# Kernel tuning notes

Measured on AMD Instinct MI355X. Metric: run time of the kernel, lower is better.

The kernel has to match this reference:

```python
import jax, jax.numpy as jnp
import numpy as np

N_NODES = 100_000
N_EDGES = 1_600_000
IN_C, OUT_C = 128, 64


def setup_inputs() -> dict:
    key = jax.random.key(0)
    k1, k2, k3, k4 = jax.random.split(key, 4)
    x = jax.random.normal(k1, (N_NODES, IN_C), dtype=jnp.float32)
    # xavier_uniform with relu gain sqrt(2)
    gain = float(np.sqrt(2.0))
    bound = gain * float(np.sqrt(6.0 / (IN_C + OUT_C)))
    weight = jax.random.uniform(k2, (IN_C, OUT_C), minval=-bound, maxval=bound, dtype=jnp.float32)
    bias = jnp.zeros((OUT_C,), dtype=jnp.float32)
    src = jax.random.randint(k3, (N_EDGES,), 0, N_NODES, dtype=jnp.int32)
    dst = jax.random.randint(k4, (N_EDGES,), 0, N_NODES, dtype=jnp.int32)
    return {"x": x, "weight": weight, "bias": bias, "src": src, "dst": dst}


def reference(x, weight, bias, src, dst):
    # DGL GraphConv, norm='both'.
    n = x.shape[0]
    ones = jnp.ones(src.shape, dtype=x.dtype)
    deg_out = jax.ops.segment_sum(ones, src, num_segments=n)  # source out-degree
    deg_in = jax.ops.segment_sum(ones, dst, num_segments=n)   # destination in-degree
    norm_src = jnp.maximum(deg_out, 1.0) ** -0.5
    norm_dst = jnp.maximum(deg_in, 1.0) ** -0.5
    h = x * norm_src[:, None]          # [N, IN]
    # in_channels > out_channels: apply weight before aggregation (DGL fast path)
    h = h @ weight                      # [N, OUT]
    msg = h[src]                        # [E, OUT] gather
    agg = jax.ops.segment_sum(msg, dst, num_segments=n)  # [N, OUT] scatter-add
    return agg * norm_dst[:, None] + bias
```

## Files before the change

kernel.cpp:

```cpp
#include <hip/hip_runtime.h>
#include <hip/hip_bf16.h>

#define N_NODES 100000
#define N_EDGES 1600000
#define IN_C    128
#define OUT_C   64

#define SLOT_W 48
#define CAP    47

#define GEMM_BLK 512
#define FILL_BLK ((N_EDGES + 255) / 256)

typedef __bf16 bf16x8 __attribute__((ext_vector_type(8)));
typedef float  f32x4  __attribute__((ext_vector_type(4)));

#define DEGS_OFF  0
#define CNT_OFF   400000
#define SLOT_OFF  800000
#define H_OFF     20000000

__global__ __launch_bounds__(256) void fused_fill_gemm(
    const float* __restrict__ x, const float* __restrict__ w,
    const int* __restrict__ src, const int* __restrict__ dst,
    int* __restrict__ degs, int* __restrict__ cnt, int* __restrict__ slots,
    __bf16* __restrict__ h) {
  if (blockIdx.x >= GEMM_BLK) {
    const int i = (blockIdx.x - GEMM_BLK) * 256 + threadIdx.x;
    if (i < N_EDGES) {
      const int s = src[i];
      const int d = dst[i];
      atomicAdd(&degs[s], 1);
      const int pos = atomicAdd(&cnt[d], 1);
      if (pos < CAP) slots[d * SLOT_W + pos] = s;
    }
    return;
  }

  const int lane = threadIdx.x & 63;
  const int l15 = lane & 15;
  const int q = lane >> 4;
  const int wave = blockIdx.x * 4 + (threadIdx.x >> 6);
  const int n_waves = GEMM_BLK * 4;
  const int n_groups = N_NODES / 16;

  bf16x8 bfrag[4][4];
#pragma unroll
  for (int kc = 0; kc < 4; ++kc) {
#pragma unroll
    for (int t = 0; t < 4; ++t) {
      bf16x8 tmp;
#pragma unroll
      for (int j = 0; j < 8; ++j)
        tmp[j] = (__bf16)w[(kc * 32 + q * 8 + j) * OUT_C + t * 16 + l15];
      bfrag[kc][t] = tmp;
    }
  }

  for (int g = wave; g < n_groups; g += n_waves) {
    const int n0 = g * 16;
    const float* xp = x + (long)(n0 + l15) * IN_C + q * 8;

    f32x4 acc[4];
#pragma unroll
    for (int t = 0; t < 4; ++t) {
      f32x4 z = {0.f, 0.f, 0.f, 0.f};
      acc[t] = z;
    }

#pragma unroll
    for (int kc = 0; kc < 4; ++kc) {
      f32x4 u = *(const f32x4*)(xp + kc * 32);
      f32x4 v = *(const f32x4*)(xp + kc * 32 + 4);
      bf16x8 a;
#pragma unroll
      for (int j = 0; j < 4; ++j) {
        a[j] = (__bf16)u[j];
        a[4 + j] = (__bf16)v[j];
      }
#pragma unroll
      for (int t = 0; t < 4; ++t)
        acc[t] = __builtin_amdgcn_mfma_f32_16x16x32_bf16(a, bfrag[kc][t], acc[t], 0, 0, 0);
    }

#pragma unroll
    for (int r = 0; r < 4; ++r) {
      const int row = n0 + q * 4 + r;
#pragma unroll
      for (int t = 0; t < 4; ++t)
        h[(long)row * OUT_C + t * 16 + l15] = (__bf16)acc[t][r];
    }
  }
}

__global__ __launch_bounds__(256) void scale_kernel(
    __bf16* __restrict__ h, const int* __restrict__ degs) {
  int tid = blockIdx.x * 256 + threadIdx.x;
  if (tid >= N_NODES * 8) return;
  int n = tid >> 3;
  int c8 = (tid & 7) * 8;
  int d = degs[n];
  float s = rsqrtf((float)(d < 1 ? 1 : d));
  bf16x8* p = (bf16x8*)(h + (long)n * OUT_C + c8);
  bf16x8 v = *p;
#pragma unroll
  for (int k = 0; k < 8; ++k) v[k] = (__bf16)((float)v[k] * s);
  *p = v;
}

__global__ __launch_bounds__(256) void aggregate_kernel(
    const __bf16* __restrict__ h, const int* __restrict__ cnt,
    const int* __restrict__ slots, const float* __restrict__ bias,
    float* __restrict__ out) {
  const int node = blockIdx.x * 4 + (threadIdx.x >> 6);
  if (node >= N_NODES) return;
  const int lane = threadIdx.x & 63;
  const int eg = lane >> 3;
  const int c8 = (lane & 7) * 8;

  const int c = cnt[node];
  const float ndv = rsqrtf((float)(c < 1 ? 1 : c));
  const int end = c < CAP ? c : CAP;
  const int* sl = slots + (long)node * SLOT_W;

  float acc[8];
#pragma unroll
  for (int k = 0; k < 8; ++k) acc[k] = 0.f;

  for (int j = 0; j < end; j += 8) {
    const int e = j + eg;
    if (e < end) {
      const int s = sl[e];
      bf16x8 v = *(const bf16x8*)(h + (long)s * OUT_C + c8);
#pragma unroll
      for (int k = 0; k < 8; ++k) acc[k] += (float)v[k];
    }
  }

#pragma unroll
  for (int mask = 8; mask <= 32; mask <<= 1) {
#pragma unroll
    for (int k = 0; k < 8; ++k)
      acc[k] += __shfl_xor(acc[k], mask, 64);
  }

  if (lane < 8) {
    f32x4 r0, r1;
#pragma unroll
    for (int k = 0; k < 4; ++k) {
      r0[k] = acc[k] * ndv + bias[c8 + k];
      r1[k] = acc[4 + k] * ndv + bias[c8 + 4 + k];
    }
    float* op = out + (long)node * OUT_C + c8;
    *(f32x4*)op = r0;
    *(f32x4*)(op + 4) = r1;
  }
}

extern "C" void kernel_launch(void* const* d_in, const int* in_sizes, int n_in,
                              void* d_out, int out_size, void* d_ws, size_t ws_size,
                              hipStream_t stream) {
  const float* x    = (const float*)d_in[0];
  const float* w    = (const float*)d_in[1];
  const float* bias = (const float*)d_in[2];
  const int*   src  = (const int*)d_in[3];
  const int*   dst  = (const int*)d_in[4];
  float* out = (float*)d_out;

  char* ws = (char*)d_ws;
  int*    degs  = (int*)(ws + DEGS_OFF);
  int*    cnt   = (int*)(ws + CNT_OFF);
  int*    slots = (int*)(ws + SLOT_OFF);
  __bf16* h     = (__bf16*)(ws + H_OFF);

  hipMemsetAsync(ws, 0, 2 * N_NODES * sizeof(int), stream);

  fused_fill_gemm<<<GEMM_BLK + FILL_BLK, 256, 0, stream>>>(
      x, w, src, dst, degs, cnt, slots, h);

  scale_kernel<<<(N_NODES * 8 + 255) / 256, 256, 0, stream>>>(h, degs);

  aggregate_kernel<<<(N_NODES + 3) / 4, 256, 0, stream>>>(
      h, cnt, slots, bias, out);
}
```

Measured before the change: 300.4 us.

## Split h into column planes and partition atomics and gathers by XCD

h is stored as four 16-column planes, so each aggregation block gathers 32-byte slices from one 3.2MB plane. Blocks are mapped so that each XCD works on a single plane, which lets the plane stay resident in that XCD's L2. The edge fill now runs as 1024 blocks looping over all edges, and each block group only does atomics for nodes in its own XCD range. This is meant to keep atomics local to one L2. The cost is that every fill block reads the full src/dst arrays (8x more index traffic), and aggregation rereads the slot lists four times, once per plane.

```diff
diff --git a/kernel.cpp b/kernel.cpp
--- a/kernel.cpp
+++ b/kernel.cpp
@@ -9,8 +9,17 @@
 #define SLOT_W 48
 #define CAP    47
 
+#define NXCD       8
+#define NODES_PER_XCD 12500
+
 #define GEMM_BLK 512
-#define FILL_BLK ((N_EDGES + 255) / 256)
+#define FILL_BLK 1024
+
+#define PLANE_ELEMS (N_NODES * 16)
+
+#define AGG_Q    1563
+#define AGG_GRID (AGG_Q * 8)
+#define AGG_IDX  3125
 
 typedef __bf16 bf16x8 __attribute__((ext_vector_type(8)));
 typedef float  f32x4  __attribute__((ext_vector_type(4)));
@@ -26,13 +35,19 @@
     int* __restrict__ degs, int* __restrict__ cnt, int* __restrict__ slots,
     __bf16* __restrict__ h) {
   if (blockIdx.x >= GEMM_BLK) {
-    const int i = (blockIdx.x - GEMM_BLK) * 256 + threadIdx.x;
-    if (i < N_EDGES) {
+    const int f = blockIdx.x - GEMM_BLK;
+    const int g = f & 7;
+    const int j = f >> 3;
+    const int nlo = g * NODES_PER_XCD;
+    const int nhi = nlo + NODES_PER_XCD;
+    for (int i = j * 256 + threadIdx.x; i < N_EDGES; i += 128 * 256) {
       const int s = src[i];
       const int d = dst[i];
-      atomicAdd(&degs[s], 1);
-      const int pos = atomicAdd(&cnt[d], 1);
-      if (pos < CAP) slots[d * SLOT_W + pos] = s;
+      if (d >= nlo && d < nhi) {
+        const int pos = atomicAdd(&cnt[d], 1);
+        if (pos < CAP) slots[d * SLOT_W + pos] = s;
+      }
+      if (s >= nlo && s < nhi) atomicAdd(&degs[s], 1);
     }
     return;
   }
@@ -88,7 +103,7 @@
       const int row = n0 + q * 4 + r;
 #pragma unroll
       for (int t = 0; t < 4; ++t)
-        h[(long)row * OUT_C + t * 16 + l15] = (__bf16)acc[t][r];
+        h[(long)t * PLANE_ELEMS + row * 16 + l15] = (__bf16)acc[t][r];
     }
   }
 }
@@ -96,64 +111,79 @@
 __global__ __launch_bounds__(256) void scale_kernel(
     __bf16* __restrict__ h, const int* __restrict__ degs) {
   int tid = blockIdx.x * 256 + threadIdx.x;
-  if (tid >= N_NODES * 8) return;
-  int n = tid >> 3;
-  int c8 = (tid & 7) * 8;
+  if (tid >= 4 * N_NODES * 2) return;
+  int p = tid / (N_NODES * 2);
+  int r = tid % (N_NODES * 2);
+  int n = r >> 1;
+  int hh = r & 1;
   int d = degs[n];
   float s = rsqrtf((float)(d < 1 ? 1 : d));
-  bf16x8* p = (bf16x8*)(h + (long)n * OUT_C + c8);
-  bf16x8 v = *p;
+  bf16x8* ptr = (bf16x8*)(h + (long)p * PLANE_ELEMS + n * 16 + hh * 8);
+  bf16x8 v = *ptr;
 #pragma unroll
   for (int k = 0; k < 8; ++k) v[k] = (__bf16)((float)v[k] * s);
-  *p = v;
+  *ptr = v;
 }
 
 __global__ __launch_bounds__(256) void aggregate_kernel(
     const __bf16* __restrict__ h, const int* __restrict__ cnt,
     const int* __restrict__ slots, const float* __restrict__ bias,
     float* __restrict__ out) {
-  const int node = blockIdx.x * 4 + (threadIdx.x >> 6);
-  if (node >= N_NODES) return;
+  const int gb = blockIdx.x;
+  const int r8 = gb & 7;
+  const int p = r8 >> 1;
+  const int idx = (gb >> 3) * 2 + (r8 & 1);
+  if (idx >= AGG_IDX) return;
+  const int wv = threadIdx.x >> 6;
   const int lane = threadIdx.x & 63;
-  const int eg = lane >> 3;
-  const int c8 = (lane & 7) * 8;
-
-  const int c = cnt[node];
-  const float ndv = rsqrtf((float)(c < 1 ? 1 : c));
-  const int end = c < CAP ? c : CAP;
-  const int* sl = slots + (long)node * SLOT_W;
-
-  float acc[8];
-#pragma unroll
-  for (int k = 0; k < 8; ++k) acc[k] = 0.f;
-
-  for (int j = 0; j < end; j += 8) {
-    const int e = j + eg;
-    if (e < end) {
-      const int s = sl[e];
-      bf16x8 v = *(const bf16x8*)(h + (long)s * OUT_C + c8);
-#pragma unroll
-      for (int k = 0; k < 8; ++k) acc[k] += (float)v[k];
-    }
-  }
-
-#pragma unroll
-  for (int mask = 8; mask <= 32; mask <<= 1) {
-#pragma unroll
-    for (int k = 0; k < 8; ++k)
-      acc[k] += __shfl_xor(acc[k], mask, 64);
-  }
-
-  if (lane < 8) {
-    f32x4 r0, r1;
-#pragma unroll
-    for (int k = 0; k < 4; ++k) {
-      r0[k] = acc[k] * ndv + bias[c8 + k];
-      r1[k] = acc[4 + k] * ndv + bias[c8 + 4 + k];
-    }
-    float* op = out + (long)node * OUT_C + c8;
-    *(f32x4*)op = r0;
-    *(f32x4*)(op + 4) = r1;
+  const int e_i = lane >> 1;
+  const int hh = lane & 1;
+  const __bf16* hp = h + (long)p * PLANE_ELEMS + hh * 8;
+
+  float bv[8];
+#pragma unroll
+  for (int k = 0; k < 8; ++k) bv[k] = bias[p * 16 + hh * 8 + k];
+
+  const int nodeBase = idx * 32 + wv * 8;
+  for (int nn = 0; nn < 8; ++nn) {
+    const int node = nodeBase + nn;
+    const int c = cnt[node];
+    const int end = c < CAP ? c : CAP;
+    const int* sl = slots + (long)node * SLOT_W;
+
+    float acc[8];
+#pragma unroll
+    for (int k = 0; k < 8; ++k) acc[k] = 0.f;
+
+    for (int j = 0; j < end; j += 32) {
+      const int e = j + e_i;
+      if (e < end) {
+        const int s = sl[e];
+        bf16x8 v = *(const bf16x8*)(hp + (long)s * 16);
+#pragma unroll
+        for (int k = 0; k < 8; ++k) acc[k] += (float)v[k];
+      }
+    }
+
+#pragma unroll
+    for (int mask = 2; mask <= 32; mask <<= 1) {
+#pragma unroll
+      for (int k = 0; k < 8; ++k)
+        acc[k] += __shfl_xor(acc[k], mask, 64);
+    }
+
+    if (lane < 2) {
+      const float ndv = rsqrtf((float)(c < 1 ? 1 : c));
+      f32x4 r0, r1;
+#pragma unroll
+      for (int k = 0; k < 4; ++k) {
+        r0[k] = acc[k] * ndv + bv[k];
+        r1[k] = acc[4 + k] * ndv + bv[4 + k];
+      }
+      float* op = out + (long)node * OUT_C + p * 16 + hh * 8;
+      *(f32x4*)op = r0;
+      *(f32x4*)(op + 4) = r1;
+    }
   }
 }
 
@@ -178,8 +208,7 @@
   fused_fill_gemm<<<GEMM_BLK + FILL_BLK, 256, 0, stream>>>(
       x, w, src, dst, degs, cnt, slots, h);
 
-  scale_kernel<<<(N_NODES * 8 + 255) / 256, 256, 0, stream>>>(h, degs);
-
-  aggregate_kernel<<<(N_NODES + 3) / 4, 256, 0, stream>>>(
-      h, cnt, slots, bias, out);
-}
+  scale_kernel<<<(4 * N_NODES * 2 + 255) / 256, 256, 0, stream>>>(h, degs);
+
+  aggregate_kernel<<<AGG_GRID, 256, 0, stream>>>(h, cnt, slots, bias, out);
+}
```

Result: slower. 427.5 us (+42.3%).

## Split slot fill in two halves and overlap second half with partial aggregation

Applied to the files above, without the earlier changes.

The destination-slot fill is split. The first half of the edges is filled alongside the GEMM. The second half is filled in the same launch as a partial aggregation over the slots the first half already wrote, and a final kernel adds the remaining slots, normalizes and adds bias. The aim is to hide the atomic fill cost behind the gather work. The trade-off is an extra kernel, an extra pass over the output (read-modify-write), and a snapshot copy of the counts. Capped slot ordering is nondeterministic, but it was already nondeterministic before.

```diff
diff --git a/kernel.cpp b/kernel.cpp
--- a/kernel.cpp
+++ b/kernel.cpp
@@ -3,36 +3,42 @@
 
 #define N_NODES 100000
 #define N_EDGES 1600000
+#define E1END   800000
 #define IN_C    128
 #define OUT_C   64
 
 #define SLOT_W 48
 #define CAP    47
 
-#define GEMM_BLK 512
-#define FILL_BLK ((N_EDGES + 255) / 256)
+#define GEMM_BLK  512
+#define FILL1_BLK 2048
+#define FILL2_BLK 1024
+#define AGG_BLK   25000
 
 typedef __bf16 bf16x8 __attribute__((ext_vector_type(8)));
 typedef float  f32x4  __attribute__((ext_vector_type(4)));
 
 #define DEGS_OFF  0
 #define CNT_OFF   400000
-#define SLOT_OFF  800000
-#define H_OFF     20000000
-
-__global__ __launch_bounds__(256) void fused_fill_gemm(
+#define CNT1_OFF  800000
+#define SLOT_OFF  1200000
+#define H_OFF     20400000
+
+__global__ __launch_bounds__(256) void fused_gemm_fill1(
     const float* __restrict__ x, const float* __restrict__ w,
     const int* __restrict__ src, const int* __restrict__ dst,
     int* __restrict__ degs, int* __restrict__ cnt, int* __restrict__ slots,
     __bf16* __restrict__ h) {
   if (blockIdx.x >= GEMM_BLK) {
-    const int i = (blockIdx.x - GEMM_BLK) * 256 + threadIdx.x;
-    if (i < N_EDGES) {
+    const int f = blockIdx.x - GEMM_BLK;
+    for (int i = f * 256 + threadIdx.x; i < N_EDGES; i += FILL1_BLK * 256) {
       const int s = src[i];
-      const int d = dst[i];
       atomicAdd(&degs[s], 1);
-      const int pos = atomicAdd(&cnt[d], 1);
-      if (pos < CAP) slots[d * SLOT_W + pos] = s;
+      if (i < E1END) {
+        const int d = dst[i];
+        const int pos = atomicAdd(&cnt[d], 1);
+        if (pos < CAP) slots[d * SLOT_W + pos] = s;
+      }
     }
     return;
   }
@@ -94,8 +100,10 @@
 }
 
 __global__ __launch_bounds__(256) void scale_kernel(
-    __bf16* __restrict__ h, const int* __restrict__ degs) {
+    __bf16* __restrict__ h, const int* __restrict__ degs,
+    const int* __restrict__ cnt, int* __restrict__ cnt1) {
   int tid = blockIdx.x * 256 + threadIdx.x;
+  if (tid < N_NODES) cnt1[tid] = cnt[tid];
   if (tid >= N_NODES * 8) return;
   int n = tid >> 3;
   int c8 = (tid & 7) * 8;
@@ -108,26 +116,84 @@
   *p = v;
 }
 
-__global__ __launch_bounds__(256) void aggregate_kernel(
+__global__ __launch_bounds__(256) void fused_fill2_aggA(
+    const int* __restrict__ src, const int* __restrict__ dst,
+    int* __restrict__ cnt, int* __restrict__ slots,
+    const __bf16* __restrict__ h, const int* __restrict__ cnt1,
+    float* __restrict__ out) {
+  if (blockIdx.x < FILL2_BLK) {
+    for (int i = E1END + blockIdx.x * 256 + threadIdx.x; i < N_EDGES;
+         i += FILL2_BLK * 256) {
+      const int s = src[i];
+      const int d = dst[i];
+      const int pos = atomicAdd(&cnt[d], 1);
+      if (pos < CAP) slots[d * SLOT_W + pos] = s;
+    }
+    return;
+  }
+
+  const int node = (blockIdx.x - FILL2_BLK) * 4 + (threadIdx.x >> 6);
+  if (node >= N_NODES) return;
+  const int lane = threadIdx.x & 63;
+  const int eg = lane >> 3;
+  const int c8 = (lane & 7) * 8;
+
+  const int c1 = cnt1[node];
+  const int end = c1 < CAP ? c1 : CAP;
+  const int* sl = slots + (long)node * SLOT_W;
+
+  float acc[8];
+#pragma unroll
+  for (int k = 0; k < 8; ++k) acc[k] = 0.f;
+
+  for (int j = 0; j < end; j += 8) {
+    const int e = j + eg;
+    if (e < end) {
+      const int s = sl[e];
+      bf16x8 v = *(const bf16x8*)(h + (long)s * OUT_C + c8);
+#pragma unroll
+      for (int k = 0; k < 8; ++k) acc[k] += (float)v[k];
+    }
+  }
+
+#pragma unroll
+  for (int mask = 8; mask <= 32; mask <<= 1) {
+#pragma unroll
+    for (int k = 0; k < 8; ++k)
+      acc[k] += __shfl_xor(acc[k], mask, 64);
+  }
+
+  if (lane < 8) {
+    f32x4 r0, r1;
+#pragma unroll
+    for (int k = 0; k < 4; ++k) { r0[k] = acc[k]; r1[k] = acc[4 + k]; }
+    float* op = out + (long)node * OUT_C + c8;
+    *(f32x4*)op = r0;
+    *(f32x4*)(op + 4) = r1;
+  }
+}
+
+__global__ __launch_bounds__(256) void aggB_finalize(
     const __bf16* __restrict__ h, const int* __restrict__ cnt,
-    const int* __restrict__ slots, const float* __restrict__ bias,
-    float* __restrict__ out) {
+    const int* __restrict__ cnt1, const int* __restrict__ slots,
+    const float* __restrict__ bias, float* __restrict__ out) {
   const int node = blockIdx.x * 4 + (threadIdx.x >> 6);
   if (node >= N_NODES) return;
   const int lane = threadIdx.x & 63;
   const int eg = lane >> 3;
   const int c8 = (lane & 7) * 8;
 
-  const int c = cnt[node];
-  const float ndv = rsqrtf((float)(c < 1 ? 1 : c));
-  const int end = c < CAP ? c : CAP;
+  const int ct = cnt[node];
+  const int c1 = cnt1[node];
+  const int start = c1 < CAP ? c1 : CAP;
+  const int end = ct < CAP ? ct : CAP;
   const int* sl = slots + (long)node * SLOT_W;
 
   float acc[8];
 #pragma unroll
   for (int k = 0; k < 8; ++k) acc[k] = 0.f;
 
-  for (int j = 0; j < end; j += 8) {
+  for (int j = start; j < end; j += 8) {
     const int e = j + eg;
     if (e < end) {
       const int s = sl[e];
@@ -145,13 +211,16 @@
   }
 
   if (lane < 8) {
+    const float ndv = rsqrtf((float)(ct < 1 ? 1 : ct));
+    float* op = out + (long)node * OUT_C + c8;
+    f32x4 p0 = *(f32x4*)op;
+    f32x4 p1 = *(f32x4*)(op + 4);
     f32x4 r0, r1;
 #pragma unroll
     for (int k = 0; k < 4; ++k) {
-      r0[k] = acc[k] * ndv + bias[c8 + k];
-      r1[k] = acc[4 + k] * ndv + bias[c8 + 4 + k];
-    }
-    float* op = out + (long)node * OUT_C + c8;
+      r0[k] = (p0[k] + acc[k]) * ndv + bias[c8 + k];
+      r1[k] = (p1[k] + acc[4 + k]) * ndv + bias[c8 + 4 + k];
+    }
     *(f32x4*)op = r0;
     *(f32x4*)(op + 4) = r1;
   }
@@ -170,16 +239,19 @@
   char* ws = (char*)d_ws;
   int*    degs  = (int*)(ws + DEGS_OFF);
   int*    cnt   = (int*)(ws + CNT_OFF);
+  int*    cnt1  = (int*)(ws + CNT1_OFF);
   int*    slots = (int*)(ws + SLOT_OFF);
   __bf16* h     = (__bf16*)(ws + H_OFF);
 
   hipMemsetAsync(ws, 0, 2 * N_NODES * sizeof(int), stream);
 
-  fused_fill_gemm<<<GEMM_BLK + FILL_BLK, 256, 0, stream>>>(
+  fused_gemm_fill1<<<GEMM_BLK + FILL1_BLK, 256, 0, stream>>>(
       x, w, src, dst, degs, cnt, slots, h);
 
-  scale_kernel<<<(N_NODES * 8 + 255) / 256, 256, 0, stream>>>(h, degs);
-
-  aggregate_kernel<<<(N_NODES + 3) / 4, 256, 0, stream>>>(
-      h, cnt, slots, bias, out);
-}
+  scale_kernel<<<(N_NODES * 8 + 255) / 256, 256, 0, stream>>>(h, degs, cnt, cnt1);
+
+  fused_fill2_aggA<<<FILL2_BLK + AGG_BLK, 256, 0, stream>>>(
+      src, dst, cnt, slots, h, cnt1, out);
+
+  aggB_finalize<<<AGG_BLK, 256, 0, stream>>>(h, cnt, cnt1, slots, bias, out);
+}
```

Result: slower. 324.9 us (+8.1%).

## Pack in-degree counter into slot records and move slot fill beside scaling

Applied to the files above, without the earlier changes.

The per-destination counter now lives in word 0 of a 48-int record, directly before that node's source slots. The atomic that reserves a slot and the aggregation's read of the count therefore touch the same cache line as the slot list. The edge pass is split in two: the GEMM kernel now overlaps only the out-degree atomics, and the slot fill runs with grid-stride loops in a kernel fused with the degree scaling. In exchange, the memset must now clear the whole record region (about 19 MB instead of 0.8 MB), and the scaling kernel's launch waits for the fill blocks' share of the device.

```diff
diff --git a/kernel.cpp b/kernel.cpp
--- a/kernel.cpp
+++ b/kernel.cpp
@@ -6,34 +6,30 @@
 #define IN_C    128
 #define OUT_C   64
 
-#define SLOT_W 48
-#define CAP    47
+#define REC_W 48
+#define CAP   47
 
-#define GEMM_BLK 512
-#define FILL_BLK ((N_EDGES + 255) / 256)
+#define GEMM_BLK  512
+#define DEG_BLK   1024
+#define FILL_BLK  2048
+#define SCALE_BLK 3125
+#define AGG_BLK   25000
 
 typedef __bf16 bf16x8 __attribute__((ext_vector_type(8)));
 typedef float  f32x4  __attribute__((ext_vector_type(4)));
 
 #define DEGS_OFF  0
-#define CNT_OFF   400000
-#define SLOT_OFF  800000
-#define H_OFF     20000000
+#define REC_OFF   400000
+#define H_OFF     19600000
 
-__global__ __launch_bounds__(256) void fused_fill_gemm(
+__global__ __launch_bounds__(256) void fused_gemm_degs(
     const float* __restrict__ x, const float* __restrict__ w,
-    const int* __restrict__ src, const int* __restrict__ dst,
-    int* __restrict__ degs, int* __restrict__ cnt, int* __restrict__ slots,
-    __bf16* __restrict__ h) {
+    const int* __restrict__ src,
+    int* __restrict__ degs, __bf16* __restrict__ h) {
   if (blockIdx.x >= GEMM_BLK) {
-    const int i = (blockIdx.x - GEMM_BLK) * 256 + threadIdx.x;
-    if (i < N_EDGES) {
-      const int s = src[i];
-      const int d = dst[i];
-      atomicAdd(&degs[s], 1);
-      const int pos = atomicAdd(&cnt[d], 1);
-      if (pos < CAP) slots[d * SLOT_W + pos] = s;
-    }
+    const int f = blockIdx.x - GEMM_BLK;
+    for (int i = f * 256 + threadIdx.x; i < N_EDGES; i += DEG_BLK * 256)
+      atomicAdd(&degs[src[i]], 1);
     return;
   }
 
@@ -93,14 +89,27 @@
   }
 }
 
-__global__ __launch_bounds__(256) void scale_kernel(
-    __bf16* __restrict__ h, const int* __restrict__ degs) {
-  int tid = blockIdx.x * 256 + threadIdx.x;
-  if (tid >= N_NODES * 8) return;
-  int n = tid >> 3;
-  int c8 = (tid & 7) * 8;
-  int d = degs[n];
-  float s = rsqrtf((float)(d < 1 ? 1 : d));
+__global__ __launch_bounds__(256) void fused_fill_scale(
+    const int* __restrict__ src, const int* __restrict__ dst,
+    int* __restrict__ rec, __bf16* __restrict__ h,
+    const int* __restrict__ degs) {
+  if (blockIdx.x < FILL_BLK) {
+    for (int i = blockIdx.x * 256 + threadIdx.x; i < N_EDGES;
+         i += FILL_BLK * 256) {
+      const int s = src[i];
+      const int d = dst[i];
+      int* r = rec + d * REC_W;
+      const int pos = atomicAdd(r, 1);
+      if (pos < CAP) r[1 + pos] = s;
+    }
+    return;
+  }
+
+  const int t = (blockIdx.x - FILL_BLK) * 256 + threadIdx.x;
+  const int n = t >> 3;
+  const int c8 = (t & 7) * 8;
+  const int d = degs[n];
+  const float s = rsqrtf((float)(d < 1 ? 1 : d));
   bf16x8* p = (bf16x8*)(h + (long)n * OUT_C + c8);
   bf16x8 v = *p;
 #pragma unroll
@@ -109,19 +118,19 @@
 }
 
 __global__ __launch_bounds__(256) void aggregate_kernel(
-    const __bf16* __restrict__ h, const int* __restrict__ cnt,
-    const int* __restrict__ slots, const float* __restrict__ bias,
-    float* __restrict__ out) {
+    const __bf16* __restrict__ h, const int* __restrict__ rec,
+    const float* __restrict__ bias, float* __restrict__ out) {
   const int node = blockIdx.x * 4 + (threadIdx.x >> 6);
   if (node >= N_NODES) return;
   const int lane = threadIdx.x & 63;
   const int eg = lane >> 3;
   const int c8 = (lane & 7) * 8;
 
-  const int c = cnt[node];
+  const int* r = rec + (long)node * REC_W;
+  const int c = r[0];
   const float ndv = rsqrtf((float)(c < 1 ? 1 : c));
   const int end = c < CAP ? c : CAP;
-  const int* sl = slots + (long)node * SLOT_W;
+  const int* sl = r + 1;
 
   float acc[8];
 #pragma unroll
@@ -168,18 +177,16 @@
   float* out = (float*)d_out;
 
   char* ws = (char*)d_ws;
-  int*    degs  = (int*)(ws + DEGS_OFF);
-  int*    cnt   = (int*)(ws + CNT_OFF);
-  int*    slots = (int*)(ws + SLOT_OFF);
-  __bf16* h     = (__bf16*)(ws + H_OFF);
+  int*    degs = (int*)(ws + DEGS_OFF);
+  int*    rec  = (int*)(ws + REC_OFF);
+  __bf16* h    = (__bf16*)(ws + H_OFF);
 
-  hipMemsetAsync(ws, 0, 2 * N_NODES * sizeof(int), stream);
+  hipMemsetAsync(ws, 0, REC_OFF + N_NODES * REC_W * sizeof(int), stream);
 
-  fused_fill_gemm<<<GEMM_BLK + FILL_BLK, 256, 0, stream>>>(
-      x, w, src, dst, degs, cnt, slots, h);
+  fused_gemm_degs<<<GEMM_BLK + DEG_BLK, 256, 0, stream>>>(x, w, src, degs, h);
 
-  scale_kernel<<<(N_NODES * 8 + 255) / 256, 256, 0, stream>>>(h, degs);
+  fused_fill_scale<<<FILL_BLK + SCALE_BLK, 256, 0, stream>>>(
+      src, dst, rec, h, degs);
 
-  aggregate_kernel<<<(N_NODES + 3) / 4, 256, 0, stream>>>(
-      h, cnt, slots, bias, out);
+  aggregate_kernel<<<AGG_BLK, 256, 0, stream>>>(h, rec, bias, out);
 }
```

After: 304.0 us. Within noise of the previous version (+1.2%).
